# Optimization experiments

Measured on AMD Instinct MI355X. Metric: run time of the kernel, lower is better.

## Reference

```python
import jax, jax.numpy as jnp
import numpy as np

N = 50000
E = 800000
H = 128
K = 4
BN_EPS = 1e-5


def _cheb_norm(edge_index):
    # PyG ChebConv with normalization='sym', lambda_max=2.0:
    # L_hat = 2L/lambda_max - I = -D^{-1/2} A D^{-1/2}
    src, dst = edge_index[0], edge_index[1]
    deg = jax.ops.segment_sum(jnp.ones((E,), jnp.float32), src, num_segments=N)
    dinv = jnp.where(deg > 0, jax.lax.rsqrt(jnp.maximum(deg, 1.0)), 0.0)
    return -dinv[src] * dinv[dst]  # [E]


def _cheb_conv(x, src, dst, w, W, b):
    # Chebyshev recursion: Tx0=x, Tx1=L_hat x, Txk = 2 L_hat Tx_{k-1} - Tx_{k-2}
    def prop(h):
        return jax.ops.segment_sum(h[src] * w[:, None], dst, num_segments=N)
    Tx0 = x
    out = Tx0 @ W[0]
    Tx1 = prop(Tx0)
    out = out + Tx1 @ W[1]
    for k in range(2, W.shape[0]):
        Tx2 = 2.0 * prop(Tx1) - Tx0
        out = out + Tx2 @ W[k]
        Tx0, Tx1 = Tx1, Tx2
    return out + b


def _bn(h, gamma, beta):
    # BatchNorm1d, training mode: biased batch stats over nodes
    m = h.mean(axis=0)
    v = h.var(axis=0)
    return (h - m) * jax.lax.rsqrt(v + BN_EPS) * gamma + beta


def setup_inputs() -> dict:
    key = jax.random.key(0)
    ks = jax.random.split(key, 8)
    x = jax.random.normal(ks[0], (N, 3), jnp.float32)
    edge_index = jax.random.randint(ks[1], (2, E), 0, N, jnp.int64)
    s1 = 1.0 / np.sqrt(3)
    s2 = 1.0 / np.sqrt(H)
    d = {
        'x': x,
        'edge_index': edge_index,
        'W1': jax.random.normal(ks[2], (K, 3, H), jnp.float32) * s1,
        'b1': jnp.zeros((H,), jnp.float32),
        'W2': jax.random.normal(ks[3], (K, H, H), jnp.float32) * s2,
        'b2': jnp.zeros((H,), jnp.float32),
        'W3': jax.random.normal(ks[4], (K, H, H), jnp.float32) * s2,
        'b3': jnp.zeros((H,), jnp.float32),
        'W4': jax.random.normal(ks[5], (K, H, H), jnp.float32) * s2,
        'b4': jnp.zeros((H,), jnp.float32),
        'g1': jnp.ones((H,), jnp.float32), 'be1': jnp.zeros((H,), jnp.float32),
        'g2': jnp.ones((H,), jnp.float32), 'be2': jnp.zeros((H,), jnp.float32),
        'g3': jnp.ones((H,), jnp.float32), 'be3': jnp.zeros((H,), jnp.float32),
    }
    return d


def reference(x, edge_index, W1, b1, W2, b2, W3, b3, W4, b4, g1, be1, g2, be2, g3, be3):
    src, dst = edge_index[0], edge_index[1]
    w = _cheb_norm(edge_index)
    h = _bn(jax.nn.leaky_relu(_cheb_conv(x, src, dst, w, W1, b1)), g1, be1)
    h = _bn(jax.nn.leaky_relu(_cheb_conv(h, src, dst, w, W2, b2)), g2, be2)
    h = _bn(jax.nn.relu(_cheb_conv(h, src, dst, w, W3, b3)), g3, be3)
    h = _cheb_conv(h, src, dst, w, W4, b4)
    # F.normalize(p=2, dim=1)
    nrm = jnp.sqrt(jnp.sum(h * h, axis=1, keepdims=True))
    return h / jnp.maximum(nrm, 1e-12)
```

## Files before the change

kernel.cpp:

```cpp
#include <hip/hip_runtime.h>
#include <hip/hip_fp16.h>

#define NN 50000
#define NE 800000
#define HD 128
#define NSL 128
#define SLE (NE / NSL)
#define PW  12500

typedef __attribute__((ext_vector_type(8))) short short8;
typedef __attribute__((ext_vector_type(4))) float f32x4;
typedef __attribute__((ext_vector_type(4))) unsigned u32x4;

__device__ inline unsigned bf2pack(float lo, float hi) {
    unsigned a = __float_as_uint(lo); a = (a + 0x7fffu + ((a >> 16) & 1u)) >> 16;
    unsigned b = __float_as_uint(hi); b = (b + 0x7fffu + ((b >> 16) & 1u)) >> 16;
    return a | (b << 16);
}

__device__ inline float edgw(unsigned p) {
    return __half2float(__ushort_as_half((unsigned short)(p >> 16)));
}

__global__ __launch_bounds__(256) void k_hist(const int* __restrict__ ei,
                                              unsigned* __restrict__ phist) {
    __shared__ unsigned hist[PW];
    int b = blockIdx.x;
    int a = b >> 8;
    int s = (b & 255) >> 1;
    int c = b & 1;
    int tid = threadIdx.x;
    for (int i = tid; i < PW; i += 256) hist[i] = 0u;
    __syncthreads();
    const int* arr = ei + a * NE + s * SLE;
    int lo = c * 25000;
    for (int i = tid; i < SLE; i += 256) {
        int v = arr[i] - lo;
        if ((unsigned)v < 25000u)
            atomicAdd(&hist[v >> 1], 1u << ((v & 1) * 16));
    }
    __syncthreads();
    unsigned* dst = phist + (size_t)b * PW;
    for (int i = tid; i < PW; i += 256) dst[i] = hist[i];
}

__global__ __launch_bounds__(256) void k_hreduce(const unsigned* __restrict__ phist,
                                                 float* __restrict__ dinv,
                                                 int* __restrict__ cnt,
                                                 unsigned* __restrict__ pre) {
    int idx = blockIdx.x * 256 + threadIdx.x;
    if (idx >= 50000) return;
    int a = idx / 25000;
    int gw = idx % 25000;
    int c = gw / PW;
    int w = gw % PW;
    unsigned accLo = 0, accHi = 0;
    for (int s = 0; s < NSL; s++) {
        unsigned p = phist[(size_t)(((a * NSL + s) * 2 + c)) * PW + w];
        if (a == 1) pre[(size_t)s * 25000 + gw] = accLo | (accHi << 16);
        accLo += p & 0xffffu;
        accHi += p >> 16;
    }
    int b0 = c * 25000 + 2 * w;
    if (a == 0) {
        dinv[b0]     = accLo ? rsqrtf((float)accLo) : 0.0f;
        dinv[b0 + 1] = accHi ? rsqrtf((float)accHi) : 0.0f;
    } else {
        cnt[b0]     = (int)accLo;
        cnt[b0 + 1] = (int)accHi;
    }
}

__global__ __launch_bounds__(1024) void k_scan1(const int* __restrict__ cnt,
                                                int* __restrict__ rowptr,
                                                int* __restrict__ bsum) {
    __shared__ int s[1024];
    int tid = threadIdx.x;
    int gid = blockIdx.x * 1024 + tid;
    int v = (gid < NN) ? cnt[gid] : 0;
    s[tid] = v;
    __syncthreads();
    for (int off = 1; off < 1024; off <<= 1) {
        int t = 0;
        if (tid >= off) t = s[tid - off];
        __syncthreads();
        s[tid] += t;
        __syncthreads();
    }
    if (gid < NN) rowptr[gid] = s[tid] - v;
    if (tid == 1023) bsum[blockIdx.x] = s[1023];
}

__global__ void k_scan2(const int* __restrict__ bsum, int* __restrict__ boff,
                        int nb, int* __restrict__ rowptr) {
    int lane = threadIdx.x;
    int v = (lane < nb) ? bsum[lane] : 0;
    int s = v;
    #pragma unroll
    for (int off = 1; off < 64; off <<= 1) {
        int t = __shfl_up(s, off, 64);
        if (lane >= off) s += t;
    }
    if (lane < nb) boff[lane] = s - v;
    if (lane == 63) rowptr[NN] = s;
}

__global__ void k_scan3(int* __restrict__ rowptr, const int* __restrict__ boff) {
    int i = blockIdx.x * 256 + threadIdx.x;
    if (i < NN) rowptr[i] += boff[i >> 10];
}

__global__ __launch_bounds__(256) void k_fill2(const int* __restrict__ ei,
                                               const float* __restrict__ dinv,
                                               const int* __restrict__ rowptr,
                                               const unsigned* __restrict__ pre,
                                               unsigned* __restrict__ edg) {
    __shared__ unsigned rank[PW];
    int b = blockIdx.x;
    int s = b >> 1;
    int c = b & 1;
    int tid = threadIdx.x;
    for (int i = tid; i < PW; i += 256) rank[i] = 0u;
    __syncthreads();
    int lo = c * 25000;
    const unsigned* preS = pre + (size_t)s * 25000 + c * PW;
    for (int i = tid; i < SLE; i += 256) {
        int e = s * SLE + i;
        int d = ei[NE + e];
        int v = d - lo;
        if ((unsigned)v < 25000u) {
            int src = ei[e];
            int w = v >> 1;
            int sh = (v & 1) * 16;
            unsigned r = atomicAdd(&rank[w], 1u << sh);
            r = (r >> sh) & 0xffffu;
            unsigned pw = (preS[w] >> sh) & 0xffffu;
            int pos = rowptr[d] + (int)pw + (int)r;
            unsigned short hw = __half_as_ushort(__float2half(-dinv[src] * dinv[d]));
            edg[pos] = (unsigned)src | ((unsigned)hw << 16);
        }
    }
}

__global__ __launch_bounds__(128) void k_prop3(const float* __restrict__ h,
                        const float* __restrict__ sub,
                        const int* __restrict__ rowptr, const unsigned* __restrict__ edg,
                        float* __restrict__ out) {
    int node = blockIdx.x * 128 + threadIdx.x;
    if (node >= NN) return;
    int e0 = rowptr[node], e1 = rowptr[node + 1];
    float a0 = 0.f, a1 = 0.f, a2 = 0.f;
    float c0 = 0.f, c1 = 0.f, c2 = 0.f;
    int e = e0;
    for (; e + 4 <= e1; e += 4) {
        unsigned p0 = edg[e], p1 = edg[e + 1], p2 = edg[e + 2], p3 = edg[e + 3];
        int s0 = (int)(p0 & 0xffffu) * 3, s1 = (int)(p1 & 0xffffu) * 3;
        int s2 = (int)(p2 & 0xffffu) * 3, s3 = (int)(p3 & 0xffffu) * 3;
        float x0 = h[s0], y0 = h[s0 + 1], z0 = h[s0 + 2];
        float x1 = h[s1], y1 = h[s1 + 1], z1 = h[s1 + 2];
        float x2 = h[s2], y2 = h[s2 + 1], z2 = h[s2 + 2];
        float x3 = h[s3], y3 = h[s3 + 1], z3 = h[s3 + 2];
        float w0 = edgw(p0), w1 = edgw(p1), w2 = edgw(p2), w3 = edgw(p3);
        a0 = fmaf(w0, x0, a0); a1 = fmaf(w0, y0, a1); a2 = fmaf(w0, z0, a2);
        c0 = fmaf(w1, x1, c0); c1 = fmaf(w1, y1, c1); c2 = fmaf(w1, z1, c2);
        a0 = fmaf(w2, x2, a0); a1 = fmaf(w2, y2, a1); a2 = fmaf(w2, z2, a2);
        c0 = fmaf(w3, x3, c0); c1 = fmaf(w3, y3, c1); c2 = fmaf(w3, z3, c2);
    }
    if (e < e1) {
        unsigned p0 = edg[e];
        unsigned p1 = (e + 1 < e1) ? edg[e + 1] : 0u;
        unsigned p2 = (e + 2 < e1) ? edg[e + 2] : 0u;
        int s0 = (int)(p0 & 0xffffu) * 3, s1 = (int)(p1 & 0xffffu) * 3;
        int s2 = (int)(p2 & 0xffffu) * 3;
        float x0 = h[s0], y0 = h[s0 + 1], z0 = h[s0 + 2];
        float x1 = h[s1], y1 = h[s1 + 1], z1 = h[s1 + 2];
        float x2 = h[s2], y2 = h[s2 + 1], z2 = h[s2 + 2];
        float w0 = edgw(p0), w1 = edgw(p1), w2 = edgw(p2);
        a0 = fmaf(w0, x0, a0); a1 = fmaf(w0, y0, a1); a2 = fmaf(w0, z0, a2);
        c0 = fmaf(w1, x1, c0); c1 = fmaf(w1, y1, c1); c2 = fmaf(w1, z1, c2);
        a0 = fmaf(w2, x2, a0); a1 = fmaf(w2, y2, a1); a2 = fmaf(w2, z2, a2);
    }
    a0 += c0; a1 += c1; a2 += c2;
    if (sub) {
        a0 = 2.f * a0 - sub[node * 3 + 0];
        a1 = 2.f * a1 - sub[node * 3 + 1];
        a2 = 2.f * a2 - sub[node * 3 + 2];
    }
    out[node * 3 + 0] = a0;
    out[node * 3 + 1] = a1;
    out[node * 3 + 2] = a2;
}

#define ACC8(acc, u, v)                                               \
    acc[0] = fmaf(v, __uint_as_float(u[0] << 16), acc[0]);            \
    acc[1] = fmaf(v, __uint_as_float(u[0] & 0xffff0000u), acc[1]);    \
    acc[2] = fmaf(v, __uint_as_float(u[1] << 16), acc[2]);            \
    acc[3] = fmaf(v, __uint_as_float(u[1] & 0xffff0000u), acc[3]);    \
    acc[4] = fmaf(v, __uint_as_float(u[2] << 16), acc[4]);            \
    acc[5] = fmaf(v, __uint_as_float(u[2] & 0xffff0000u), acc[5]);    \
    acc[6] = fmaf(v, __uint_as_float(u[3] << 16), acc[6]);            \
    acc[7] = fmaf(v, __uint_as_float(u[3] & 0xffff0000u), acc[7]);

__global__ __launch_bounds__(256) void k_prop_pl(
        const unsigned short* __restrict__ h, const unsigned short* __restrict__ sub,
        const int* __restrict__ rowptr, const unsigned* __restrict__ edg,
        unsigned short* __restrict__ out) {
    int B = blockIdx.x;
    int xcd = B & 7;
    int c = xcd >> 1;
    int half = xcd & 1;
    int g = B >> 3;
    int n = (half * 392 + g) * 64 + (threadIdx.x >> 2);
    if (n >= NN) return;
    int lane4 = threadIdx.x & 3;
    int sl = lane4 * 8;
    int base = (threadIdx.x & 63) & ~3;
    const unsigned short* hp = h + (size_t)c * (NN * 32);
    int e0 = rowptr[n], e1 = rowptr[n + 1];
    float a[8] = {0, 0, 0, 0, 0, 0, 0, 0};
    float b[8] = {0, 0, 0, 0, 0, 0, 0, 0};
    int e = e0;
    for (; e + 8 <= e1; e += 8) {
        uint2 pp = *(const uint2*)(edg + e + lane4 * 2);
        unsigned q0 = __shfl(pp.x, base + 0, 64);
        unsigned q1 = __shfl(pp.y, base + 0, 64);
        unsigned q2 = __shfl(pp.x, base + 1, 64);
        unsigned q3 = __shfl(pp.y, base + 1, 64);
        unsigned q4 = __shfl(pp.x, base + 2, 64);
        unsigned q5 = __shfl(pp.y, base + 2, 64);
        unsigned q6 = __shfl(pp.x, base + 3, 64);
        unsigned q7 = __shfl(pp.y, base + 3, 64);
        u32x4 u0 = *(const u32x4*)(hp + (q0 & 0xffffu) * 32 + sl);
        u32x4 u1 = *(const u32x4*)(hp + (q1 & 0xffffu) * 32 + sl);
        u32x4 u2 = *(const u32x4*)(hp + (q2 & 0xffffu) * 32 + sl);
        u32x4 u3 = *(const u32x4*)(hp + (q3 & 0xffffu) * 32 + sl);
        u32x4 u4 = *(const u32x4*)(hp + (q4 & 0xffffu) * 32 + sl);
        u32x4 u5 = *(const u32x4*)(hp + (q5 & 0xffffu) * 32 + sl);
        u32x4 u6 = *(const u32x4*)(hp + (q6 & 0xffffu) * 32 + sl);
        u32x4 u7 = *(const u32x4*)(hp + (q7 & 0xffffu) * 32 + sl);
        float v0 = edgw(q0), v1 = edgw(q1), v2 = edgw(q2), v3 = edgw(q3);
        float v4 = edgw(q4), v5 = edgw(q5), v6 = edgw(q6), v7 = edgw(q7);
        ACC8(a, u0, v0)
        ACC8(b, u1, v1)
        ACC8(a, u2, v2)
        ACC8(b, u3, v3)
        ACC8(a, u4, v4)
        ACC8(b, u5, v5)
        ACC8(a, u6, v6)
        ACC8(b, u7, v7)
    }
    int rem = e1 - e;
    if (rem > 0) {
        uint2 pp = *(const uint2*)(edg + e + lane4 * 2);
        unsigned q0 = __shfl(pp.x, base + 0, 64);
        unsigned q1 = __shfl(pp.y, base + 0, 64);
        unsigned q2 = __shfl(pp.x, base + 1, 64);
        unsigned q3 = __shfl(pp.y, base + 1, 64);
        unsigned q4 = __shfl(pp.x, base + 2, 64);
        unsigned q5 = __shfl(pp.y, base + 2, 64);
        unsigned q6 = __shfl(pp.x, base + 3, 64);
        unsigned q7 = __shfl(pp.y, base + 3, 64);
        q1 = (rem > 1) ? q1 : 0u;
        q2 = (rem > 2) ? q2 : 0u;
        q3 = (rem > 3) ? q3 : 0u;
        q4 = (rem > 4) ? q4 : 0u;
        q5 = (rem > 5) ? q5 : 0u;
        q6 = (rem > 6) ? q6 : 0u;
        q7 = 0u;
        u32x4 u0 = *(const u32x4*)(hp + (q0 & 0xffffu) * 32 + sl);
        u32x4 u1 = *(const u32x4*)(hp + (q1 & 0xffffu) * 32 + sl);
        u32x4 u2 = *(const u32x4*)(hp + (q2 & 0xffffu) * 32 + sl);
        u32x4 u3 = *(const u32x4*)(hp + (q3 & 0xffffu) * 32 + sl);
        u32x4 u4 = *(const u32x4*)(hp + (q4 & 0xffffu) * 32 + sl);
        u32x4 u5 = *(const u32x4*)(hp + (q5 & 0xffffu) * 32 + sl);
        u32x4 u6 = *(const u32x4*)(hp + (q6 & 0xffffu) * 32 + sl);
        u32x4 u7 = *(const u32x4*)(hp + (q7 & 0xffffu) * 32 + sl);
        float v0 = edgw(q0), v1 = edgw(q1), v2 = edgw(q2), v3 = edgw(q3);
        float v4 = edgw(q4), v5 = edgw(q5), v6 = edgw(q6), v7 = edgw(q7);
        ACC8(a, u0, v0)
        ACC8(b, u1, v1)
        ACC8(a, u2, v2)
        ACC8(b, u3, v3)
        ACC8(a, u4, v4)
        ACC8(b, u5, v5)
        ACC8(a, u6, v6)
        ACC8(b, u7, v7)
    }
    float r[8];
    #pragma unroll
    for (int q = 0; q < 8; q++) r[q] = a[q] + b[q];
    if (sub) {
        u32x4 su = __builtin_nontemporal_load(
            (const u32x4*)(sub + (size_t)c * (NN * 32) + n * 32 + sl));
        float s[8];
        s[0] = __uint_as_float(su[0] << 16); s[1] = __uint_as_float(su[0] & 0xffff0000u);
        s[2] = __uint_as_float(su[1] << 16); s[3] = __uint_as_float(su[1] & 0xffff0000u);
        s[4] = __uint_as_float(su[2] << 16); s[5] = __uint_as_float(su[2] & 0xffff0000u);
        s[6] = __uint_as_float(su[3] << 16); s[7] = __uint_as_float(su[3] & 0xffff0000u);
        #pragma unroll
        for (int q = 0; q < 8; q++) r[q] = 2.f * r[q] - s[q];
    }
    u32x4 o;
    o[0] = bf2pack(r[0], r[1]);
    o[1] = bf2pack(r[2], r[3]);
    o[2] = bf2pack(r[4], r[5]);
    o[3] = bf2pack(r[6], r[7]);
    __builtin_nontemporal_store(o, (u32x4*)(out + (size_t)c * (NN * 32) + n * 32 + sl));
}

__global__ void k_wconv_all(const float* __restrict__ W2, const float* __restrict__ W3,
                            const float* __restrict__ W4, unsigned short* __restrict__ Wb) {
    int gidx = blockIdx.x * 256 + threadIdx.x;
    int which = gidx >> 16;
    int idx = gidx & 65535;
    const float* W = which == 0 ? W2 : (which == 1 ? W3 : W4);
    int slot = idx >> 9;
    int lane = (idx >> 3) & 63;
    int j = idx & 7;
    int wg = slot >> 4;
    int t = slot & 15;
    int w = wg >> 1;
    int g = wg & 1;
    int k = t * 32 + (lane >> 4) * 8 + j;
    int col = w * 32 + g * 16 + (lane & 15);
    unsigned u = __float_as_uint(W[k * HD + col]);
    Wb[which * 65536 + idx] = (unsigned short)((u + 0x7fffu + ((u >> 16) & 1u)) >> 16);
}

__global__ __launch_bounds__(256) void k_gemmM(
        const unsigned short* __restrict__ A0, const unsigned short* __restrict__ A1,
        const unsigned short* __restrict__ A2, const unsigned short* __restrict__ A3,
        const unsigned short* __restrict__ Wb, const float* __restrict__ bias,
        float* __restrict__ outF, int act, float* __restrict__ gpart) {
    __shared__ unsigned short Asm[16 * 64 * 8];
    __shared__ float sred[64];
    const int tid = threadIdx.x;
    const int w = tid >> 6;
    const int lane = tid & 63;
    const int l15 = lane & 15;
    const int quad = lane >> 4;

    short8 Bf[16][2];
    #pragma unroll
    for (int t = 0; t < 16; t++) {
        #pragma unroll
        for (int g = 0; g < 2; g++) {
            int slot = (w * 2 + g) * 16 + t;
            Bf[t][g] = *(const short8*)(Wb + slot * 512 + lane * 8);
        }
    }
    float bcol[2];
    bcol[0] = bias[w * 32 + l15];
    bcol[1] = bias[w * 32 + 16 + l15];

    const unsigned short* Ap[4] = {A0, A1, A2, A3};
    float bnP[2] = {0.f, 0.f}, bnQ[2] = {0.f, 0.f};

    for (int tile = blockIdx.x; tile < NN / 16; tile += gridDim.x) {
        int r0 = tile * 16;
        __syncthreads();
        #pragma unroll
        for (int i = 0; i < 4; i++) {
            int idx = i * 256 + tid;
            int s = idx >> 6;
            int ln = idx & 63;
            const unsigned short* src = Ap[s >> 2] + (size_t)(s & 3) * (NN * 32)
                                        + (r0 + (ln & 15)) * 32 + (ln >> 4) * 8;
            *(uint4*)&Asm[idx * 8] = *(const uint4*)src;
        }
        __syncthreads();
        f32x4 acc0 = {0.f, 0.f, 0.f, 0.f};
        f32x4 acc1 = {0.f, 0.f, 0.f, 0.f};
        #pragma unroll
        for (int s = 0; s < 16; s++) {
            short8 af = *(const short8*)&Asm[(s * 64 + lane) * 8];
            acc0 = __builtin_amdgcn_mfma_f32_16x16x32_bf16(af, Bf[s][0], acc0, 0, 0, 0);
            acc1 = __builtin_amdgcn_mfma_f32_16x16x32_bf16(af, Bf[s][1], acc1, 0, 0, 0);
        }
        if (act == 3) {
            float vv0[4], vv1[4], rs[4];
            #pragma unroll
            for (int reg = 0; reg < 4; reg++) {
                float v0 = acc0[reg] + bcol[0];
                float v1 = acc1[reg] + bcol[1];
                vv0[reg] = v0; vv1[reg] = v1;
                float s2 = v0 * v0 + v1 * v1;
                s2 += __shfl_xor(s2, 1);
                s2 += __shfl_xor(s2, 2);
                s2 += __shfl_xor(s2, 4);
                s2 += __shfl_xor(s2, 8);
                rs[reg] = s2;
            }
            if (l15 == 0) {
                #pragma unroll
                for (int reg = 0; reg < 4; reg++)
                    sred[w * 16 + quad * 4 + reg] = rs[reg];
            }
            __syncthreads();
            #pragma unroll
            for (int reg = 0; reg < 4; reg++) {
                int row16 = quad * 4 + reg;
                float tot = sred[row16] + sred[16 + row16]
                          + sred[32 + row16] + sred[48 + row16];
                float sc = 1.f / fmaxf(sqrtf(tot), 1e-12f);
                int row = r0 + row16;
                outF[row * HD + w * 32 + l15] = vv0[reg] * sc;
                outF[row * HD + w * 32 + 16 + l15] = vv1[reg] * sc;
            }
        } else {
            #pragma unroll
            for (int reg = 0; reg < 4; reg++) {
                int row = r0 + quad * 4 + reg;
                float v0 = acc0[reg] + bcol[0];
                float v1 = acc1[reg] + bcol[1];
                if (act == 1) {
                    v0 = v0 > 0.f ? v0 : 0.01f * v0;
                    v1 = v1 > 0.f ? v1 : 0.01f * v1;
                } else if (act == 2) {
                    v0 = v0 > 0.f ? v0 : 0.f;
                    v1 = v1 > 0.f ? v1 : 0.f;
                }
                outF[row * HD + w * 32 + l15] = v0;
                outF[row * HD + w * 32 + 16 + l15] = v1;
                bnP[0] += v0; bnQ[0] += v0 * v0;
                bnP[1] += v1; bnQ[1] += v1 * v1;
            }
        }
    }
    if (gpart) {
        #pragma unroll
        for (int g = 0; g < 2; g++) {
            float p = bnP[g], q = bnQ[g];
            p += __shfl_xor(p, 16); p += __shfl_xor(p, 32);
            q += __shfl_xor(q, 16); q += __shfl_xor(q, 32);
            if (quad == 0) {
                int col = w * 32 + g * 16 + l15;
                gpart[col * 512 + blockIdx.x] = p;
                gpart[(128 + col) * 512 + blockIdx.x] = q;
            }
        }
    }
}

__global__ __launch_bounds__(256) void k_gemm1(
        const float* __restrict__ T0, const float* __restrict__ T1,
        const float* __restrict__ T2, const float* __restrict__ T3,
        const float* __restrict__ W, const float* __restrict__ bias,
        float* __restrict__ out, float* __restrict__ gpart) {
    __shared__ float Ws[12 * 128];
    __shared__ float red[512];
    int t = threadIdx.x;
    for (int i = t; i < 12 * 128; i += 256) Ws[i] = W[i];
    __syncthreads();
    int f = t & 127;
    int half = t >> 7;
    float bs = bias[f];
    float bP = 0.f, bQ = 0.f;
    int r0 = blockIdx.x * 98;
    int r1 = r0 + 98;
    if (r1 > NN) r1 = NN;
    const float* Ts[4] = {T0, T1, T2, T3};
    for (int n = r0 + half; n < r1; n += 2) {
        float acc = bs;
        #pragma unroll
        for (int c = 0; c < 12; c++) {
            float tv = Ts[c / 3][n * 3 + (c % 3)];
            acc = fmaf(tv, Ws[c * 128 + f], acc);
        }
        acc = acc > 0.f ? acc : 0.01f * acc;
        out[n * HD + f] = acc;
        bP += acc;
        bQ += acc * acc;
    }
    red[t] = bP;
    red[256 + t] = bQ;
    __syncthreads();
    if (t < 128) {
        gpart[t * 512 + blockIdx.x] = red[t] + red[t + 128];
        gpart[(128 + t) * 512 + blockIdx.x] = red[256 + t] + red[256 + t + 128];
    }
}

__global__ __launch_bounds__(128) void k_bnredfin(const float* __restrict__ gpart,
                                                  const float* __restrict__ g,
                                                  const float* __restrict__ be,
                                                  float* __restrict__ ss) {
    __shared__ float sm[2];
    int f = blockIdx.x;
    int wave = threadIdx.x >> 6;
    int lane = threadIdx.x & 63;
    const float* src = gpart + (size_t)(f + wave * 128) * 512;
    float s = 0.f;
    #pragma unroll
    for (int i = 0; i < 8; i++) s += src[i * 64 + lane];
    #pragma unroll
    for (int off = 32; off > 0; off >>= 1) s += __shfl_xor(s, off);
    if (lane == 0) sm[wave] = s;
    __syncthreads();
    if (threadIdx.x == 0) {
        float mean = sm[0] * (1.0f / NN);
        float var = sm[1] * (1.0f / NN) - mean * mean;
        float sc = g[f] * rsqrtf(var + 1e-5f);
        ss[f] = sc;
        ss[128 + f] = be[f] - mean * sc;
    }
}

__global__ void k_bncvt_pl(const float* __restrict__ h, const float* __restrict__ ss,
                           unsigned short* __restrict__ out) {
    int idx = blockIdx.x * 256 + threadIdx.x;
    if (idx < NN * 16) {
        int n = idx >> 4;
        int p = (idx >> 2) & 3;
        int q = idx & 3;
        const float4* hf = (const float4*)h;
        float4 v0 = hf[n * 32 + p * 8 + q * 2];
        float4 v1 = hf[n * 32 + p * 8 + q * 2 + 1];
        const float4* s4 = (const float4*)ss;
        float4 c0 = s4[p * 8 + q * 2];
        float4 c1 = s4[p * 8 + q * 2 + 1];
        float4 d0 = s4[32 + p * 8 + q * 2];
        float4 d1 = s4[32 + p * 8 + q * 2 + 1];
        v0.x = fmaf(v0.x, c0.x, d0.x); v0.y = fmaf(v0.y, c0.y, d0.y);
        v0.z = fmaf(v0.z, c0.z, d0.z); v0.w = fmaf(v0.w, c0.w, d0.w);
        v1.x = fmaf(v1.x, c1.x, d1.x); v1.y = fmaf(v1.y, c1.y, d1.y);
        v1.z = fmaf(v1.z, c1.z, d1.z); v1.w = fmaf(v1.w, c1.w, d1.w);
        uint4 o;
        o.x = bf2pack(v0.x, v0.y);
        o.y = bf2pack(v0.z, v0.w);
        o.z = bf2pack(v1.x, v1.y);
        o.w = bf2pack(v1.z, v1.w);
        ((uint4*)out)[(size_t)p * (NN * 4) + n * 4 + q] = o;
    }
}

extern "C" void kernel_launch(void* const* d_in, const int* in_sizes, int n_in,
                              void* d_out, int out_size, void* d_ws, size_t ws_size,
                              hipStream_t stream) {
    const float* x  = (const float*)d_in[0];
    const int*   ei = (const int*)d_in[1];
    const float* W1 = (const float*)d_in[2];
    const float* b1 = (const float*)d_in[3];
    const float* W2 = (const float*)d_in[4];
    const float* b2 = (const float*)d_in[5];
    const float* W3 = (const float*)d_in[6];
    const float* b3 = (const float*)d_in[7];
    const float* W4 = (const float*)d_in[8];
    const float* b4 = (const float*)d_in[9];
    const float* g1 = (const float*)d_in[10];
    const float* be1 = (const float*)d_in[11];
    const float* g2 = (const float*)d_in[12];
    const float* be2 = (const float*)d_in[13];
    const float* g3 = (const float*)d_in[14];
    const float* be3 = (const float*)d_in[15];
    float* outp = (float*)d_out;

    char* base = (char*)d_ws;
    size_t off = 0;
    auto alloc = [&](size_t bytes) -> void* {
        void* p = base + off;
        off += (bytes + 255) & ~(size_t)255;
        return p;
    };
    float* dinv  = (float*)alloc(NN * 4);
    int*   cnt   = (int*)  alloc(NN * 4);
    int*   rowptr= (int*)  alloc((NN + 1) * 4);
    int*   bsum  = (int*)  alloc(64 * 4);
    int*   boff  = (int*)  alloc(64 * 4);
    float* ss    = (float*)alloc(256 * 4);
    float* gpart = (float*)alloc(256 * 512 * 4);
    unsigned short* Wb = (unsigned short*)alloc(3 * 512 * 128 * 2);
    unsigned* edg = (unsigned*)alloc((size_t)(NE + 8) * 4);
    float* T3a   = (float*)alloc(NN * 3 * 4);
    float* T3b   = (float*)alloc(NN * 3 * 4);
    float* T3c   = (float*)alloc(NN * 3 * 4);
    float* F0    = (float*)alloc((size_t)NN * HD * 4);
    unsigned short* Bb0 = (unsigned short*)alloc((size_t)NN * HD * 2);
    unsigned short* Bb1 = (unsigned short*)alloc((size_t)NN * HD * 2);
    unsigned short* Bb2 = (unsigned short*)alloc((size_t)NN * HD * 2);
    unsigned short* Bb3 = (unsigned short*)alloc((size_t)NN * HD * 2);

    unsigned* pre   = (unsigned*)F0;
    unsigned* phist = (unsigned*)Bb0;

    const int gN = (NN + 255) / 256;
    const int gP3 = (NN + 127) / 128;
    const int nb = (NN + 1023) / 1024;

    k_hist<<<512, 256, 0, stream>>>(ei, phist);
    k_hreduce<<<(50000 + 255) / 256, 256, 0, stream>>>(phist, dinv, cnt, pre);
    k_scan1<<<nb, 1024, 0, stream>>>(cnt, rowptr, bsum);
    k_scan2<<<1, 64, 0, stream>>>(bsum, boff, nb, rowptr);
    k_scan3<<<gN, 256, 0, stream>>>(rowptr, boff);
    k_fill2<<<256, 256, 0, stream>>>(ei, dinv, rowptr, pre, edg);
    k_wconv_all<<<768, 256, 0, stream>>>(W2, W3, W4, Wb);

    const int gPP = 8 * 392;
    const int gG = 512;
    const int gCvt = NN * 16 / 256;
    unsigned short* Wb2 = Wb;
    unsigned short* Wb3 = Wb + 65536;
    unsigned short* Wb4 = Wb + 131072;

    k_prop3<<<gP3, 128, 0, stream>>>(x, nullptr, rowptr, edg, T3a);
    k_prop3<<<gP3, 128, 0, stream>>>(T3a, x, rowptr, edg, T3b);
    k_prop3<<<gP3, 128, 0, stream>>>(T3b, T3a, rowptr, edg, T3c);
    k_gemm1<<<512, 256, 0, stream>>>(x, T3a, T3b, T3c, W1, b1, F0, gpart);
    k_bnredfin<<<128, 128, 0, stream>>>(gpart, g1, be1, ss);
    k_bncvt_pl<<<gCvt, 256, 0, stream>>>(F0, ss, Bb0);

    k_prop_pl<<<gPP, 256, 0, stream>>>(Bb0, nullptr, rowptr, edg, Bb1);
    k_prop_pl<<<gPP, 256, 0, stream>>>(Bb1, Bb0, rowptr, edg, Bb2);
    k_prop_pl<<<gPP, 256, 0, stream>>>(Bb2, Bb1, rowptr, edg, Bb3);
    k_gemmM<<<gG, 256, 0, stream>>>(Bb0, Bb1, Bb2, Bb3, Wb2, b2, F0, 1, gpart);
    k_bnredfin<<<128, 128, 0, stream>>>(gpart, g2, be2, ss);
    k_bncvt_pl<<<gCvt, 256, 0, stream>>>(F0, ss, Bb0);

    k_prop_pl<<<gPP, 256, 0, stream>>>(Bb0, nullptr, rowptr, edg, Bb1);
    k_prop_pl<<<gPP, 256, 0, stream>>>(Bb1, Bb0, rowptr, edg, Bb2);
    k_prop_pl<<<gPP, 256, 0, stream>>>(Bb2, Bb1, rowptr, edg, Bb3);
    k_gemmM<<<gG, 256, 0, stream>>>(Bb0, Bb1, Bb2, Bb3, Wb3, b3, F0, 2, gpart);
    k_bnredfin<<<128, 128, 0, stream>>>(gpart, g3, be3, ss);
    k_bncvt_pl<<<gCvt, 256, 0, stream>>>(F0, ss, Bb0);

    k_prop_pl<<<gPP, 256, 0, stream>>>(Bb0, nullptr, rowptr, edg, Bb1);
    k_prop_pl<<<gPP, 256, 0, stream>>>(Bb1, Bb0, rowptr, edg, Bb2);
    k_prop_pl<<<gPP, 256, 0, stream>>>(Bb2, Bb1, rowptr, edg, Bb3);
    k_gemmM<<<gG, 256, 0, stream>>>(Bb0, Bb1, Bb2, Bb3, Wb4, b4, outp, 3, nullptr);

    (void)n_in; (void)in_sizes; (void)out_size; (void)ws_size;
}
```

Baseline: 544.8 us.

## Process nodes in degree-sorted order to balance per-wave work in propagation

Builds a counting-sort permutation of nodes by in-degree (capped at 63) during the CSR scan, and the propagation kernels now take node ids from this permutation. Lanes in a wave then handle nodes of similar degree, which cuts divergence and idle lanes in the gather loops. The cost is an extra small kernel, an extra indirection per node, and scattered output writes and rowptr reads that lose the old sequential node locality.

After: 614.1 us. 1.13x slower.

```diff
diff --git a/kernel.cpp b/kernel.cpp
--- a/kernel.cpp
+++ b/kernel.cpp
@@ -47,7 +47,9 @@
 __global__ __launch_bounds__(256) void k_hreduce(const unsigned* __restrict__ phist,
                                                  float* __restrict__ dinv,
                                                  int* __restrict__ cnt,
-                                                 unsigned* __restrict__ pre) {
+                                                 unsigned* __restrict__ pre,
+                                                 int* __restrict__ dhist) {
+    if (blockIdx.x == 0 && threadIdx.x < 64) dhist[threadIdx.x] = 0;
     int idx = blockIdx.x * 256 + threadIdx.x;
     if (idx >= 50000) return;
     int a = idx / 25000;
@@ -73,13 +75,17 @@
 
 __global__ __launch_bounds__(1024) void k_scan1(const int* __restrict__ cnt,
                                                 int* __restrict__ rowptr,
-                                                int* __restrict__ bsum) {
+                                                int* __restrict__ bsum,
+                                                int* __restrict__ dhist) {
     __shared__ int s[1024];
+    __shared__ int dh[64];
     int tid = threadIdx.x;
     int gid = blockIdx.x * 1024 + tid;
     int v = (gid < NN) ? cnt[gid] : 0;
     s[tid] = v;
-    __syncthreads();
+    if (tid < 64) dh[tid] = 0;
+    __syncthreads();
+    if (gid < NN) atomicAdd(&dh[v < 63 ? v : 63], 1);
     for (int off = 1; off < 1024; off <<= 1) {
         int t = 0;
         if (tid >= off) t = s[tid - off];
@@ -89,10 +95,12 @@
     }
     if (gid < NN) rowptr[gid] = s[tid] - v;
     if (tid == 1023) bsum[blockIdx.x] = s[1023];
+    if (tid < 64 && dh[tid]) atomicAdd(&dhist[tid], dh[tid]);
 }
 
 __global__ void k_scan2(const int* __restrict__ bsum, int* __restrict__ boff,
-                        int nb, int* __restrict__ rowptr) {
+                        int nb, int* __restrict__ rowptr,
+                        const int* __restrict__ dhist, int* __restrict__ gbase) {
     int lane = threadIdx.x;
     int v = (lane < nb) ? bsum[lane] : 0;
     int s = v;
@@ -103,11 +111,40 @@
     }
     if (lane < nb) boff[lane] = s - v;
     if (lane == 63) rowptr[NN] = s;
+    int d = dhist[lane];
+    int sd = d;
+    #pragma unroll
+    for (int off = 1; off < 64; off <<= 1) {
+        int t = __shfl_up(sd, off, 64);
+        if (lane >= off) sd += t;
+    }
+    gbase[lane] = sd - d;
 }
 
 __global__ void k_scan3(int* __restrict__ rowptr, const int* __restrict__ boff) {
     int i = blockIdx.x * 256 + threadIdx.x;
     if (i < NN) rowptr[i] += boff[i >> 10];
+}
+
+__global__ __launch_bounds__(256) void k_permbuild(const int* __restrict__ cnt,
+                                                   int* __restrict__ gbase,
+                                                   int* __restrict__ perm) {
+    __shared__ int lcnt[64];
+    __shared__ int lbase[64];
+    int tid = threadIdx.x;
+    if (tid < 64) lcnt[tid] = 0;
+    __syncthreads();
+    int n = blockIdx.x * 256 + tid;
+    int r = 0, dg = 0;
+    if (n < NN) {
+        int v = cnt[n];
+        dg = v < 63 ? v : 63;
+        r = atomicAdd(&lcnt[dg], 1);
+    }
+    __syncthreads();
+    if (tid < 64 && lcnt[tid]) lbase[tid] = atomicAdd(&gbase[tid], lcnt[tid]);
+    __syncthreads();
+    if (n < NN) perm[lbase[dg] + r] = n;
 }
 
 __global__ __launch_bounds__(256) void k_fill2(const int* __restrict__ ei,
@@ -145,9 +182,11 @@
 __global__ __launch_bounds__(128) void k_prop3(const float* __restrict__ h,
                         const float* __restrict__ sub,
                         const int* __restrict__ rowptr, const unsigned* __restrict__ edg,
+                        const int* __restrict__ perm,
                         float* __restrict__ out) {
-    int node = blockIdx.x * 128 + threadIdx.x;
-    if (node >= NN) return;
+    int idx = blockIdx.x * 128 + threadIdx.x;
+    if (idx >= NN) return;
+    int node = perm[idx];
     int e0 = rowptr[node], e1 = rowptr[node + 1];
     float a0 = 0.f, a1 = 0.f, a2 = 0.f;
     float c0 = 0.f, c1 = 0.f, c2 = 0.f;
@@ -204,14 +243,17 @@
 __global__ __launch_bounds__(256) void k_prop_pl(
         const unsigned short* __restrict__ h, const unsigned short* __restrict__ sub,
         const int* __restrict__ rowptr, const unsigned* __restrict__ edg,
+        const int* __restrict__ perm,
         unsigned short* __restrict__ out) {
     int B = blockIdx.x;
     int xcd = B & 7;
     int c = xcd >> 1;
     int half = xcd & 1;
     int g = B >> 3;
-    int n = (half * 392 + g) * 64 + (threadIdx.x >> 2);
-    if (n >= NN) return;
+    int i = g * 64 + (threadIdx.x >> 2);
+    int si = i * 2 + half;
+    if (si >= NN) return;
+    int n = perm[si];
     int lane4 = threadIdx.x & 3;
     int sl = lane4 * 8;
     int base = (threadIdx.x & 63) & ~3;
@@ -567,6 +609,9 @@
     int*   rowptr= (int*)  alloc((NN + 1) * 4);
     int*   bsum  = (int*)  alloc(64 * 4);
     int*   boff  = (int*)  alloc(64 * 4);
+    int*   dhist = (int*)  alloc(64 * 4);
+    int*   gbase = (int*)  alloc(64 * 4);
+    int*   perm  = (int*)  alloc(NN * 4);
     float* ss    = (float*)alloc(256 * 4);
     float* gpart = (float*)alloc(256 * 512 * 4);
     unsigned short* Wb = (unsigned short*)alloc(3 * 512 * 128 * 2);
@@ -588,9 +633,10 @@
     const int nb = (NN + 1023) / 1024;
 
     k_hist<<<512, 256, 0, stream>>>(ei, phist);
-    k_hreduce<<<(50000 + 255) / 256, 256, 0, stream>>>(phist, dinv, cnt, pre);
-    k_scan1<<<nb, 1024, 0, stream>>>(cnt, rowptr, bsum);
-    k_scan2<<<1, 64, 0, stream>>>(bsum, boff, nb, rowptr);
+    k_hreduce<<<(50000 + 255) / 256, 256, 0, stream>>>(phist, dinv, cnt, pre, dhist);
+    k_scan1<<<nb, 1024, 0, stream>>>(cnt, rowptr, bsum, dhist);
+    k_scan2<<<1, 64, 0, stream>>>(bsum, boff, nb, rowptr, dhist, gbase);
+    k_permbuild<<<gN, 256, 0, stream>>>(cnt, gbase, perm);
     k_scan3<<<gN, 256, 0, stream>>>(rowptr, boff);
     k_fill2<<<256, 256, 0, stream>>>(ei, dinv, rowptr, pre, edg);
     k_wconv_all<<<768, 256, 0, stream>>>(W2, W3, W4, Wb);
@@ -602,30 +648,30 @@
     unsigned short* Wb3 = Wb + 65536;
     unsigned short* Wb4 = Wb + 131072;
 
-    k_prop3<<<gP3, 128, 0, stream>>>(x, nullptr, rowptr, edg, T3a);
-    k_prop3<<<gP3, 128, 0, stream>>>(T3a, x, rowptr, edg, T3b);
-    k_prop3<<<gP3, 128, 0, stream>>>(T3b, T3a, rowptr, edg, T3c);
+    k_prop3<<<gP3, 128, 0, stream>>>(x, nullptr, rowptr, edg, perm, T3a);
+    k_prop3<<<gP3, 128, 0, stream>>>(T3a, x, rowptr, edg, perm, T3b);
+    k_prop3<<<gP3, 128, 0, stream>>>(T3b, T3a, rowptr, edg, perm, T3c);
     k_gemm1<<<512, 256, 0, stream>>>(x, T3a, T3b, T3c, W1, b1, F0, gpart);
     k_bnredfin<<<128, 128, 0, stream>>>(gpart, g1, be1, ss);
     k_bncvt_pl<<<gCvt, 256, 0, stream>>>(F0, ss, Bb0);
 
-    k_prop_pl<<<gPP, 256, 0, stream>>>(Bb0, nullptr, rowptr, edg, Bb1);
-    k_prop_pl<<<gPP, 256, 0, stream>>>(Bb1, Bb0, rowptr, edg, Bb2);
-    k_prop_pl<<<gPP, 256, 0, stream>>>(Bb2, Bb1, rowptr, edg, Bb3);
+    k_prop_pl<<<gPP, 256, 0, stream>>>(Bb0, nullptr, rowptr, edg, perm, Bb1);
+    k_prop_pl<<<gPP, 256, 0, stream>>>(Bb1, Bb0, rowptr, edg, perm, Bb2);
+    k_prop_pl<<<gPP, 256, 0, stream>>>(Bb2, Bb1, rowptr, edg, perm, Bb3);
     k_gemmM<<<gG, 256, 0, stream>>>(Bb0, Bb1, Bb2, Bb3, Wb2, b2, F0, 1, gpart);
     k_bnredfin<<<128, 128, 0, stream>>>(gpart, g2, be2, ss);
     k_bncvt_pl<<<gCvt, 256, 0, stream>>>(F0, ss, Bb0);
 
-    k_prop_pl<<<gPP, 256, 0, stream>>>(Bb0, nullptr, rowptr, edg, Bb1);
-    k_prop_pl<<<gPP, 256, 0, stream>>>(Bb1, Bb0, rowptr, edg, Bb2);
-    k_prop_pl<<<gPP, 256, 0, stream>>>(Bb2, Bb1, rowptr, edg, Bb3);
+    k_prop_pl<<<gPP, 256, 0, stream>>>(Bb0, nullptr, rowptr, edg, perm, Bb1);
+    k_prop_pl<<<gPP, 256, 0, stream>>>(Bb1, Bb0, rowptr, edg, perm, Bb2);
+    k_prop_pl<<<gPP, 256, 0, stream>>>(Bb2, Bb1, rowptr, edg, perm, Bb3);
     k_gemmM<<<gG, 256, 0, stream>>>(Bb0, Bb1, Bb2, Bb3, Wb3, b3, F0, 2, gpart);
     k_bnredfin<<<128, 128, 0, stream>>>(gpart, g3, be3, ss);
     k_bncvt_pl<<<gCvt, 256, 0, stream>>>(F0, ss, Bb0);
 
-    k_prop_pl<<<gPP, 256, 0, stream>>>(Bb0, nullptr, rowptr, edg, Bb1);
-    k_prop_pl<<<gPP, 256, 0, stream>>>(Bb1, Bb0, rowptr, edg, Bb2);
-    k_prop_pl<<<gPP, 256, 0, stream>>>(Bb2, Bb1, rowptr, edg, Bb3);
+    k_prop_pl<<<gPP, 256, 0, stream>>>(Bb0, nullptr, rowptr, edg, perm, Bb1);
+    k_prop_pl<<<gPP, 256, 0, stream>>>(Bb1, Bb0, rowptr, edg, perm, Bb2);
+    k_prop_pl<<<gPP, 256, 0, stream>>>(Bb2, Bb1, rowptr, edg, perm, Bb3);
     k_gemmM<<<gG, 256, 0, stream>>>(Bb0, Bb1, Bb2, Bb3, Wb4, b4, outp, 3, nullptr);
 
     (void)n_in; (void)in_sizes; (void)out_size; (void)ws_size;
```
